# Performance work log

Hardware: AMD Instinct MI355X
Metric: run time of the kernel (lower is better)

## Reference

```python
import jax, jax.numpy as jnp
import numpy as np

B, N, C, P, K = 8, 65536, 96, 96, 512


def _ln(x, g, b, eps=1e-5):
    mu = x.mean(axis=-1, keepdims=True)
    var = ((x - mu) ** 2).mean(axis=-1, keepdims=True)
    return (x - mu) * jax.lax.rsqrt(var + eps) * g + b


def setup_inputs():
    key = jax.random.key(0)
    ks = jax.random.split(key, 8)
    inp = {
        "pts_feat": jax.random.normal(ks[0], (B, N, C), jnp.float32),
        "sp_idx": jax.random.randint(ks[1], (B, N), 0, K, jnp.int64),
        "all_xyz": jax.random.normal(ks[2], (B, N, 3), jnp.float32),
        # pts_proj1: Linear(3,P) -> LN -> ReLU -> Linear(P,P) -> LN
        "W1": jax.random.normal(ks[3], (3, P), jnp.float32) / np.sqrt(3.0),
        "b1": jnp.zeros((P,), jnp.float32),
        "g1": jnp.ones((P,), jnp.float32),
        "be1": jnp.zeros((P,), jnp.float32),
        "W2": jax.random.normal(ks[4], (P, P), jnp.float32) / np.sqrt(P),
        "b2": jnp.zeros((P,), jnp.float32),
        "g2": jnp.ones((P,), jnp.float32),
        "be2": jnp.zeros((P,), jnp.float32),
        # pts_proj2: Linear(2P,P) -> LN -> ReLU -> Linear(P,1,no bias) -> Sigmoid
        "W3": jax.random.normal(ks[5], (2 * P, P), jnp.float32) / np.sqrt(2.0 * P),
        "b3": jnp.zeros((P,), jnp.float32),
        "g3": jnp.ones((P,), jnp.float32),
        "be3": jnp.zeros((P,), jnp.float32),
        "W4": jax.random.normal(ks[6], (P, 1), jnp.float32) / np.sqrt(P),
        "num_sp": K,
    }
    return inp


def reference(pts_feat, sp_idx, all_xyz, W1, b1, g1, be1, W2, b2, g2, be2,
              W3, b3, g3, be3, W4, num_sp):
    Bx, Nx, Cx = pts_feat.shape
    S = Bx * num_sp  # total superpoints across batch (uniform K per batch)
    idx = (sp_idx + jnp.arange(Bx, dtype=sp_idx.dtype)[:, None] * num_sp).reshape(-1)
    xyz = all_xyz.reshape(-1, 3)
    feat = pts_feat.reshape(-1, Cx)

    # scatter_norm: unit-sphere normalize per segment
    mn = jax.ops.segment_min(xyz, idx, num_segments=S)
    mx = jax.ops.segment_max(xyz, idx, num_segments=S)
    cnt = jax.ops.segment_sum(jnp.ones((xyz.shape[0],), xyz.dtype), idx, num_segments=S)
    cnt_c = jnp.maximum(cnt, 1.0)
    center = jax.ops.segment_sum(xyz, idx, num_segments=S) / cnt_c[:, None]
    diam = (mx - mn).max(axis=1)
    pts = (xyz - center[idx]) / (diam[idx][:, None] + 0.01)

    # pts_proj1
    h = _ln(pts @ W1 + b1, g1, be1)
    h = jax.nn.relu(h)
    h = _ln(h @ W2 + b2, g2, be2)

    seg = jax.ops.segment_max(h, idx, num_segments=S)  # (S, P)
    cat = jnp.concatenate([h, seg[idx]], axis=-1)      # (B*N, 2P)

    # pts_proj2
    z = _ln(cat @ W3 + b3, g3, be3)
    z = jax.nn.relu(z)
    w = jax.nn.sigmoid(z @ W4) * 2.0                   # (B*N, 1)

    sp_feat = jax.ops.segment_sum(feat * w, idx, num_segments=S) / cnt_c[:, None] + seg
    return sp_feat.reshape(Bx, num_sp, Cx), w.reshape(Bx, Nx, 1)
```

## Files before the change

kernel.cpp:

```cpp
#include <hip/hip_runtime.h>
#include <cstdint>

#define MM 524288
#define NSEG 4096

#define WS_SCNT   0u
#define WS_CURSOR 4096u
#define WS_OFFS   8192u
#define WS_M1     12288u
#define WS_CENTER 12304u
#define WS_DIAM   24592u
#define WS_SEGF   28688u
#define WS_ZSEG   421904u
#define WS_SORTED 815120u
#define WS_H8     1339408u
#define WS_END    (WS_H8 + 25165824u)

typedef __attribute__((ext_vector_type(8))) short short8;
typedef __attribute__((ext_vector_type(4))) float f32x4;

#define WPAD 104

__device__ __forceinline__ unsigned bfr(float x) {
    unsigned u = __float_as_uint(x);
    return (u + 0x7FFFu + ((u >> 16) & 1u)) >> 16;
}
__device__ __forceinline__ float bf2f(unsigned v) {
    return __uint_as_float(v << 16);
}
union U4S8 { uint4 u; short8 s; };

__global__ void __launch_bounds__(256) k0_init(unsigned* __restrict__ ws)
{
    unsigned i = blockIdx.x * 256u + threadIdx.x;
    if (i < 8192u) ws[i] = 0u;
}

__global__ void __launch_bounds__(256) k1_count(
    const int* __restrict__ spidx, unsigned* __restrict__ scnt)
{
    __shared__ unsigned lcnt[512];
    int tid = threadIdx.x;
    for (int j = tid; j < 512; j += 256) lcnt[j] = 0u;
    __syncthreads();
    int base = blockIdx.x * 4096;
    #pragma unroll 4
    for (int it = 0; it < 16; ++it) {
        int p = base + it*256 + tid;
        atomicAdd(&lcnt[spidx[p]], 1u);
    }
    __syncthreads();
    int b = blockIdx.x >> 4;
    for (int j = tid; j < 512; j += 256)
        atomicAdd(&scnt[(b << 9) + j], lcnt[j]);
}

__global__ void __launch_bounds__(1024) k2_scan(
    const unsigned* __restrict__ scnt, unsigned* __restrict__ offs,
    const float* __restrict__ W1, const float* __restrict__ b1, float* __restrict__ m1)
{
    __shared__ unsigned sh[1024];
    int t = threadIdx.x;
    unsigned c0 = scnt[t*4+0], c1 = scnt[t*4+1], c2 = scnt[t*4+2], c3 = scnt[t*4+3];
    unsigned tot = c0 + c1 + c2 + c3;
    sh[t] = tot;
    __syncthreads();
    for (int d = 1; d < 1024; d <<= 1) {
        unsigned v = (t >= d) ? sh[t-d] : 0u;
        __syncthreads();
        sh[t] += v;
        __syncthreads();
    }
    unsigned excl = sh[t] - tot;
    offs[t*4+0] = excl;
    offs[t*4+1] = excl + c0;
    offs[t*4+2] = excl + c0 + c1;
    offs[t*4+3] = excl + c0 + c1 + c2;

    if (t == 0) {
        float Sa=0,Sb=0,Sc=0,Sd=0,Saa=0,Sbb=0,Scc=0,Sdd=0,Sab=0,Sac=0,Sad=0,Sbc=0,Sbd=0,Scd=0;
        #pragma unroll 8
        for (int j = 0; j < 96; ++j) {
            float A = W1[j], B2 = W1[96+j], C2 = W1[192+j], D = b1[j];
            Sa+=A; Sb+=B2; Sc+=C2; Sd+=D;
            Saa=fmaf(A,A,Saa); Sbb=fmaf(B2,B2,Sbb); Scc=fmaf(C2,C2,Scc); Sdd=fmaf(D,D,Sdd);
            Sab=fmaf(A,B2,Sab); Sac=fmaf(A,C2,Sac); Sad=fmaf(A,D,Sad);
            Sbc=fmaf(B2,C2,Sbc); Sbd=fmaf(B2,D,Sbd); Scd=fmaf(C2,D,Scd);
        }
        const float inv = 1.f/96.f;
        float Am=Sa*inv, Bm=Sb*inv, Cm=Sc*inv, Dm=Sd*inv;
        m1[0]=Am; m1[1]=Bm; m1[2]=Cm; m1[3]=Dm;
        m1[4]=Saa*inv-Am*Am; m1[5]=Sbb*inv-Bm*Bm; m1[6]=Scc*inv-Cm*Cm; m1[7]=Sdd*inv-Dm*Dm;
        m1[8]=Sab*inv-Am*Bm; m1[9]=Sac*inv-Am*Cm; m1[10]=Sad*inv-Am*Dm;
        m1[11]=Sbc*inv-Bm*Cm; m1[12]=Sbd*inv-Bm*Dm; m1[13]=Scd*inv-Cm*Dm;
    }
}

__global__ void __launch_bounds__(256) k3_scatter(
    const int* __restrict__ spidx, const unsigned* __restrict__ offs,
    unsigned* __restrict__ cursor, unsigned* __restrict__ sorted)
{
    __shared__ unsigned lcnt[512];
    __shared__ unsigned gbase[512];
    __shared__ unsigned short rank16[4096];
    int tid = threadIdx.x;
    for (int j = tid; j < 512; j += 256) lcnt[j] = 0u;
    __syncthreads();
    int base = blockIdx.x * 4096;
    #pragma unroll 4
    for (int it = 0; it < 16; ++it) {
        int p = base + it*256 + tid;
        unsigned r = atomicAdd(&lcnt[spidx[p]], 1u);
        rank16[it*256 + tid] = (unsigned short)r;
    }
    __syncthreads();
    int b = blockIdx.x >> 4;
    for (int j = tid; j < 512; j += 256)
        gbase[j] = atomicAdd(&cursor[(b << 9) + j], lcnt[j]);
    __syncthreads();
    #pragma unroll 4
    for (int it = 0; it < 16; ++it) {
        int p = base + it*256 + tid;
        int sl = spidx[p];
        unsigned pos = offs[(b << 9) + sl] + gbase[sl] + (unsigned)rank16[it*256 + tid];
        sorted[pos] = (unsigned)p;
    }
}

__global__ void __launch_bounds__(128) k3b_stats(
    const float* __restrict__ xyz, const unsigned* __restrict__ sorted,
    const unsigned* __restrict__ offs, const unsigned* __restrict__ scnt,
    float* __restrict__ center, float* __restrict__ diam)
{
    int s = blockIdx.x, tid = threadIdx.x;
    unsigned cnt = scnt[s], off = offs[s];
    float mnx=INFINITY, mny=INFINITY, mnz=INFINITY;
    float mxx=-INFINITY, mxy=-INFINITY, mxz=-INFINITY;
    float smx=0.f, smy=0.f, smz=0.f;
    for (unsigned r = tid; r < cnt; r += 128) {
        unsigned p = sorted[off + r];
        float x = xyz[3*p], y = xyz[3*p+1], z = xyz[3*p+2];
        mnx = fminf(mnx, x); mny = fminf(mny, y); mnz = fminf(mnz, z);
        mxx = fmaxf(mxx, x); mxy = fmaxf(mxy, y); mxz = fmaxf(mxz, z);
        smx += x; smy += y; smz += z;
    }
    #pragma unroll
    for (int m = 1; m < 64; m <<= 1) {
        mnx = fminf(mnx, __shfl_xor(mnx, m)); mny = fminf(mny, __shfl_xor(mny, m));
        mnz = fminf(mnz, __shfl_xor(mnz, m));
        mxx = fmaxf(mxx, __shfl_xor(mxx, m)); mxy = fmaxf(mxy, __shfl_xor(mxy, m));
        mxz = fmaxf(mxz, __shfl_xor(mxz, m));
        smx += __shfl_xor(smx, m); smy += __shfl_xor(smy, m); smz += __shfl_xor(smz, m);
    }
    __shared__ float cw[2][9];
    if ((tid & 63) == 0) {
        int w = tid >> 6;
        cw[w][0]=mnx; cw[w][1]=mny; cw[w][2]=mnz;
        cw[w][3]=mxx; cw[w][4]=mxy; cw[w][5]=mxz;
        cw[w][6]=smx; cw[w][7]=smy; cw[w][8]=smz;
    }
    __syncthreads();
    if (tid == 0) {
        float a0=fminf(cw[0][0],cw[1][0]), a1=fminf(cw[0][1],cw[1][1]), a2=fminf(cw[0][2],cw[1][2]);
        float b0=fmaxf(cw[0][3],cw[1][3]), b1=fmaxf(cw[0][4],cw[1][4]), b2=fmaxf(cw[0][5],cw[1][5]);
        float s0=cw[0][6]+cw[1][6], s1=cw[0][7]+cw[1][7], s2=cw[0][8]+cw[1][8];
        float cc = fmaxf((float)cnt, 1.f);
        center[s*3+0] = s0/cc; center[s*3+1] = s1/cc; center[s*3+2] = s2/cc;
        diam[s] = fmaxf(fmaxf(b0-a0, b1-a1), b2-a2);
    }
}

__global__ void __launch_bounds__(256) kT(
    const float* __restrict__ xyz, const int* __restrict__ spidx,
    const float* __restrict__ center, const float* __restrict__ diam,
    const float* __restrict__ W1, const float* __restrict__ b1,
    const float* __restrict__ g1, const float* __restrict__ be1,
    const float* __restrict__ m1, uint4* __restrict__ t8)
{
    size_t p = (size_t)blockIdx.x * 256 + threadIdx.x;
    int s = ((int)(p >> 16) << 9) + spidx[p];
    float dinv = 1.f / (diam[s] + 0.01f);
    float px = (xyz[3*p+0] - center[3*s+0]) * dinv;
    float py = (xyz[3*p+1] - center[3*s+1]) * dinv;
    float pz = (xyz[3*p+2] - center[3*s+2]) * dinv;

    float mu = fmaf(px, m1[0], fmaf(py, m1[1], fmaf(pz, m1[2], m1[3])));
    float var = fmaf(px*px, m1[4], fmaf(py*py, m1[5], fmaf(pz*pz, m1[6], m1[7])));
    var = fmaf(2.f*px*py, m1[8],  var);
    var = fmaf(2.f*px*pz, m1[9],  var);
    var = fmaf(2.f*px,    m1[10], var);
    var = fmaf(2.f*py*pz, m1[11], var);
    var = fmaf(2.f*py,    m1[12], var);
    var = fmaf(2.f*pz,    m1[13], var);
    float rs = rsqrtf(var + 1e-5f);

    #pragma unroll 4
    for (int q = 0; q < 12; ++q) {
        unsigned vv[4];
        #pragma unroll
        for (int e2 = 0; e2 < 4; ++e2) {
            int i0 = q*8 + e2*2;
            float ta = fmaf(px, W1[i0], fmaf(py, W1[96+i0], fmaf(pz, W1[192+i0], b1[i0])));
            ta = fmaxf(fmaf((ta - mu) * rs, g1[i0], be1[i0]), 0.f);
            float tb = fmaf(px, W1[i0+1], fmaf(py, W1[96+i0+1], fmaf(pz, W1[192+i0+1], b1[i0+1])));
            tb = fmaxf(fmaf((tb - mu) * rs, g1[i0+1], be1[i0+1]), 0.f);
            vv[e2] = bfr(ta) | (bfr(tb) << 16);
        }
        uint4 v; v.x = vv[0]; v.y = vv[1]; v.z = vv[2]; v.w = vv[3];
        t8[(size_t)q * MM + p] = v;
    }
}

__global__ void __launch_bounds__(256) kA_mfma(
    uint4* th8,
    const float* __restrict__ W2, const float* __restrict__ b2,
    const float* __restrict__ g2, const float* __restrict__ be2)
{
    __shared__ unsigned short wT[96*WPAD];
    __shared__ float prm[3*96];
    int tid = threadIdx.x;
    #pragma unroll 4
    for (int it = 0; it < 36; ++it) {
        int e = it*256 + tid;
        int i = e / 96;
        int j = e - i*96;
        wT[j*WPAD + i] = (unsigned short)bfr(W2[e]);
    }
    if (tid < 96) { prm[tid] = b2[tid]; prm[96+tid] = g2[tid]; prm[192+tid] = be2[tid]; }
    __syncthreads();

    int lane = tid & 63, w = tid >> 6;
    int pcol = lane & 15, g = lane >> 4;
    size_t pbase = (size_t)blockIdx.x * 256 + w * 64 + pcol;

    uint4 B0 = th8[(size_t)(0*4+g) * MM + pbase];
    uint4 B1 = th8[(size_t)(1*4+g) * MM + pbase];
    uint4 B2q = th8[(size_t)(2*4+g) * MM + pbase];

    #pragma unroll 1
    for (int t = 0; t < 4; ++t) {
        size_t p = pbase + (size_t)t * 16;
        uint4 C0 = B0, C1 = B1, C2 = B2q;
        if (t < 3) {
            size_t pn = p + 16;
            C0 = th8[(size_t)(0*4+g) * MM + pn];
            C1 = th8[(size_t)(1*4+g) * MM + pn];
            C2 = th8[(size_t)(2*4+g) * MM + pn];
        }
        U4S8 u0, u1, u2; u0.u = B0; u1.u = B1; u2.u = B2q;
        short8 bB[3] = { u0.s, u1.s, u2.s };

        f32x4 acc[6];
        #pragma unroll
        for (int nt = 0; nt < 6; ++nt) acc[nt] = (f32x4){0.f,0.f,0.f,0.f};

        #pragma unroll
        for (int ks = 0; ks < 3; ++ks) {
            #pragma unroll
            for (int nt = 0; nt < 6; ++nt) {
                const short8 aF = *(const short8*)&wT[(nt*16 + pcol)*WPAD + ks*32 + g*8];
                acc[nt] = __builtin_amdgcn_mfma_f32_16x16x32_bf16(aF, bB[ks], acc[nt], 0, 0, 0);
            }
        }

        float sum = 0.f, sq = 0.f;
        #pragma unroll
        for (int nt = 0; nt < 6; ++nt) {
            f32x4 bv = *(const f32x4*)&prm[nt*16 + g*4];
            #pragma unroll
            for (int r = 0; r < 4; ++r) {
                float v = acc[nt][r] + bv[r];
                acc[nt][r] = v;
                sum += v;
                sq = fmaf(v, v, sq);
            }
        }
        sum += __shfl_xor(sum, 16); sum += __shfl_xor(sum, 32);
        sq  += __shfl_xor(sq, 16);  sq  += __shfl_xor(sq, 32);
        float mu = sum * (1.f/96.f);
        float rs = rsqrtf(sq * (1.f/96.f) - mu*mu + 1e-5f);

        #pragma unroll
        for (int nt = 0; nt < 6; ++nt) {
            f32x4 gv  = *(const f32x4*)&prm[96  + nt*16 + g*4];
            f32x4 bev = *(const f32x4*)&prm[192 + nt*16 + g*4];
            float o0 = fmaf((acc[nt][0]-mu)*rs, gv[0], bev[0]);
            float o1 = fmaf((acc[nt][1]-mu)*rs, gv[1], bev[1]);
            float o2 = fmaf((acc[nt][2]-mu)*rs, gv[2], bev[2]);
            float o3 = fmaf((acc[nt][3]-mu)*rs, gv[3], bev[3]);
            uint2 st;
            st.x = bfr(o0) | (bfr(o1) << 16);
            st.y = bfr(o2) | (bfr(o3) << 16);
            int j0 = nt*16 + g*4;
            size_t q = (size_t)(nt*2 + (g >> 1));
            *(uint2*)((char*)th8 + (q*MM + p)*16 + (size_t)(j0 & 7)*2) = st;
        }
        B0 = C0; B1 = C1; B2q = C2;
    }
}

__global__ void __launch_bounds__(128) kB_seg(
    const unsigned short* __restrict__ h8u,
    const unsigned* __restrict__ sorted, const unsigned* __restrict__ offs,
    const unsigned* __restrict__ scnt,
    const float* __restrict__ W3, const float* __restrict__ b3,
    float* __restrict__ segf, float* __restrict__ zseg)
{
    __shared__ float lseg[96];
    int s = blockIdx.x, tid = threadIdx.x;
    unsigned cnt = scnt[s], off = offs[s];
    if (tid < 96) {
        int q = tid >> 3, e = tid & 7;
        size_t strq = (size_t)q * MM * 8 + e;
        float mx = -INFINITY;
        unsigned r = 0;
        for (; r + 4 <= cnt; r += 4) {
            unsigned p0 = sorted[off+r],   p1 = sorted[off+r+1];
            unsigned p2 = sorted[off+r+2], p3 = sorted[off+r+3];
            float a = bf2f(h8u[strq + (size_t)p0*8]);
            float b = bf2f(h8u[strq + (size_t)p1*8]);
            float c = bf2f(h8u[strq + (size_t)p2*8]);
            float d = bf2f(h8u[strq + (size_t)p3*8]);
            mx = fmaxf(mx, fmaxf(fmaxf(a,b), fmaxf(c,d)));
        }
        for (; r < cnt; ++r) {
            unsigned p0 = sorted[off+r];
            mx = fmaxf(mx, bf2f(h8u[strq + (size_t)p0*8]));
        }
        segf[(size_t)s*96 + tid] = mx;
        lseg[tid] = mx;
    }
    __syncthreads();
    if (tid < 96) {
        float acc = b3[tid];
        #pragma unroll 4
        for (int i = 0; i < 96; ++i)
            acc = fmaf(lseg[i], W3[(size_t)(96+i)*96 + tid], acc);
        zseg[(size_t)s*96 + tid] = acc;
    }
}

__global__ void __launch_bounds__(256) kC_mfma(
    const uint4* __restrict__ h8, const float* __restrict__ zseg,
    const int* __restrict__ spidx,
    const float* __restrict__ W3, const float* __restrict__ g3,
    const float* __restrict__ be3, const float* __restrict__ W4,
    float* __restrict__ w_out)
{
    __shared__ unsigned short wT[96*WPAD];
    __shared__ float prm[3*96];
    int tid = threadIdx.x;
    #pragma unroll 4
    for (int it = 0; it < 36; ++it) {
        int e = it*256 + tid;
        int i = e / 96;
        int j = e - i*96;
        wT[j*WPAD + i] = (unsigned short)bfr(W3[e]);
    }
    if (tid < 96) { prm[tid] = g3[tid]; prm[96+tid] = be3[tid]; prm[192+tid] = W4[tid]; }
    __syncthreads();

    int lane = tid & 63, w = tid >> 6;
    int pcol = lane & 15, g = lane >> 4;
    size_t pbase = (size_t)blockIdx.x * 256 + w * 64 + pcol;

    uint4 B0 = h8[(size_t)(0*4+g) * MM + pbase];
    uint4 B1 = h8[(size_t)(1*4+g) * MM + pbase];
    uint4 B2q = h8[(size_t)(2*4+g) * MM + pbase];

    #pragma unroll 1
    for (int t = 0; t < 4; ++t) {
        size_t p = pbase + (size_t)t * 16;
        uint4 C0 = B0, C1 = B1, C2 = B2q;
        if (t < 3) {
            size_t pn = p + 16;
            C0 = h8[(size_t)(0*4+g) * MM + pn];
            C1 = h8[(size_t)(1*4+g) * MM + pn];
            C2 = h8[(size_t)(2*4+g) * MM + pn];
        }
        U4S8 u0, u1, u2; u0.u = B0; u1.u = B1; u2.u = B2q;
        short8 bB[3] = { u0.s, u1.s, u2.s };

        f32x4 acc[6];
        #pragma unroll
        for (int nt = 0; nt < 6; ++nt) acc[nt] = (f32x4){0.f,0.f,0.f,0.f};

        #pragma unroll
        for (int ks = 0; ks < 3; ++ks) {
            #pragma unroll
            for (int nt = 0; nt < 6; ++nt) {
                const short8 aF = *(const short8*)&wT[(nt*16 + pcol)*WPAD + ks*32 + g*8];
                acc[nt] = __builtin_amdgcn_mfma_f32_16x16x32_bf16(aF, bB[ks], acc[nt], 0, 0, 0);
            }
        }

        int sp = spidx[p];
        int s = ((int)(p >> 16) << 9) + sp;

        float sum = 0.f, sq = 0.f;
        #pragma unroll
        for (int nt = 0; nt < 6; ++nt) {
            f32x4 zs = *(const f32x4*)&zseg[(size_t)s*96 + nt*16 + g*4];
            #pragma unroll
            for (int r = 0; r < 4; ++r) {
                float v = acc[nt][r] + zs[r];
                acc[nt][r] = v;
                sum += v;
                sq = fmaf(v, v, sq);
            }
        }
        sum += __shfl_xor(sum, 16); sum += __shfl_xor(sum, 32);
        sq  += __shfl_xor(sq, 16);  sq  += __shfl_xor(sq, 32);
        float mu = sum * (1.f/96.f);
        float rs = rsqrtf(sq * (1.f/96.f) - mu*mu + 1e-5f);

        float tt = 0.f;
        #pragma unroll
        for (int nt = 0; nt < 6; ++nt) {
            f32x4 gv  = *(const f32x4*)&prm[nt*16 + g*4];
            f32x4 bev = *(const f32x4*)&prm[96 + nt*16 + g*4];
            f32x4 w4v = *(const f32x4*)&prm[192 + nt*16 + g*4];
            #pragma unroll
            for (int r = 0; r < 4; ++r) {
                float v = fmaxf(fmaf((acc[nt][r]-mu)*rs, gv[r], bev[r]), 0.f);
                tt = fmaf(v, w4v[r], tt);
            }
        }
        tt += __shfl_xor(tt, 16); tt += __shfl_xor(tt, 32);
        if (lane < 16) w_out[p] = 2.f / (1.f + expf(-tt));

        B0 = C0; B1 = C1; B2q = C2;
    }
}

__global__ void __launch_bounds__(128) kD_pool(
    const float* __restrict__ feat, const float* __restrict__ w_out,
    const unsigned* __restrict__ sorted, const unsigned* __restrict__ offs,
    const unsigned* __restrict__ scnt, const float* __restrict__ segf,
    float* __restrict__ sp_out)
{
    int s = blockIdx.x;
    int c = threadIdx.x;
    unsigned cnt = scnt[s], off = offs[s];
    float acc = 0.f;
    unsigned r = 0;
    for (; r + 4 <= cnt; r += 4) {
        unsigned p0 = sorted[off+r],   p1 = sorted[off+r+1];
        unsigned p2 = sorted[off+r+2], p3 = sorted[off+r+3];
        float w0 = w_out[p0], w1 = w_out[p1], w2 = w_out[p2], w3 = w_out[p3];
        if (c < 96) {
            acc = fmaf(feat[(size_t)p0*96 + c], w0, acc);
            acc = fmaf(feat[(size_t)p1*96 + c], w1, acc);
            acc = fmaf(feat[(size_t)p2*96 + c], w2, acc);
            acc = fmaf(feat[(size_t)p3*96 + c], w3, acc);
        }
    }
    for (; r < cnt; ++r) {
        unsigned p0 = sorted[off+r];
        float w0 = w_out[p0];
        if (c < 96) acc = fmaf(feat[(size_t)p0*96 + c], w0, acc);
    }
    if (c < 96) {
        float cc = fmaxf((float)cnt, 1.f);
        sp_out[(size_t)s*96 + c] = acc / cc + segf[(size_t)s*96 + c];
    }
}

extern "C" void kernel_launch(void* const* d_in, const int* in_sizes, int n_in,
                              void* d_out, int out_size, void* d_ws, size_t ws_size,
                              hipStream_t stream)
{
    const float* pts_feat = (const float*)d_in[0];
    const int*   sp_idx   = (const int*)d_in[1];
    const float* xyz      = (const float*)d_in[2];
    const float* W1  = (const float*)d_in[3];
    const float* b1  = (const float*)d_in[4];
    const float* g1  = (const float*)d_in[5];
    const float* be1 = (const float*)d_in[6];
    const float* W2  = (const float*)d_in[7];
    const float* b2  = (const float*)d_in[8];
    const float* g2  = (const float*)d_in[9];
    const float* be2 = (const float*)d_in[10];
    const float* W3  = (const float*)d_in[11];
    const float* b3  = (const float*)d_in[12];
    const float* g3  = (const float*)d_in[13];
    const float* be3 = (const float*)d_in[14];
    const float* W4  = (const float*)d_in[15];

    float* out = (float*)d_out;
    float* sp_out = out;
    float* w_out  = out + (size_t)NSEG * 96;

    if (ws_size < (size_t)WS_END * 4u) return;

    unsigned* ws32   = (unsigned*)d_ws;
    unsigned* scnt   = ws32 + WS_SCNT;
    unsigned* cursor = ws32 + WS_CURSOR;
    unsigned* offs   = ws32 + WS_OFFS;
    float*    m1     = (float*)(ws32 + WS_M1);
    float*    center = (float*)(ws32 + WS_CENTER);
    float*    diam   = (float*)(ws32 + WS_DIAM);
    float*    segf   = (float*)(ws32 + WS_SEGF);
    float*    zseg   = (float*)(ws32 + WS_ZSEG);
    unsigned* sorted = ws32 + WS_SORTED;
    uint4*    th8    = (uint4*)(ws32 + WS_H8);

    k0_init<<<32, 256, 0, stream>>>(ws32);
    k1_count<<<MM/4096, 256, 0, stream>>>(sp_idx, scnt);
    k2_scan<<<1, 1024, 0, stream>>>(scnt, offs, W1, b1, m1);
    k3_scatter<<<MM/4096, 256, 0, stream>>>(sp_idx, offs, cursor, sorted);
    k3b_stats<<<NSEG, 128, 0, stream>>>(xyz, sorted, offs, scnt, center, diam);
    kT<<<MM/256, 256, 0, stream>>>(xyz, sp_idx, center, diam, W1, b1, g1, be1, m1, th8);
    kA_mfma<<<MM/256, 256, 0, stream>>>(th8, W2, b2, g2, be2);
    kB_seg<<<NSEG, 128, 0, stream>>>((const unsigned short*)th8, sorted, offs, scnt,
        W3, b3, segf, zseg);
    kC_mfma<<<MM/256, 256, 0, stream>>>(th8, zseg, sp_idx, W3, g3, be3, W4, w_out);
    kD_pool<<<NSEG, 128, 0, stream>>>(pts_feat, w_out, sorted, offs, scnt, segf, sp_out);
}
```

Before: 328.2 us.

## Fuse layer-1 and layer-2 and store hidden activations in segment-sorted order

Fuses the first projection (Linear+LN+ReLU) into the MFMA layer-2 kernel, so the intermediate bf16 activation no longer makes a round trip through global memory. Points are processed in segment-sorted order using a new per-slot segment id array written during scatter. The segment max kernel can then read contiguous, coalesced rows from h8 through LDS instead of gathering through sorted indices. The last kernel writes weights both in sorted and natural order, which adds a scattered store and an extra workspace buffer and makes the xyz reads in the fused kernel gathered.

```diff
diff --git a/kernel.cpp b/kernel.cpp
--- a/kernel.cpp
+++ b/kernel.cpp
@@ -13,7 +13,9 @@
 #define WS_SEGF   28688u
 #define WS_ZSEG   421904u
 #define WS_SORTED 815120u
-#define WS_H8     1339408u
+#define WS_SEG16  1339408u
+#define WS_WSRT   1601552u
+#define WS_H8     2125840u
 #define WS_END    (WS_H8 + 25165824u)
 
 typedef __attribute__((ext_vector_type(8))) short short8;
@@ -98,7 +100,8 @@
 
 __global__ void __launch_bounds__(256) k3_scatter(
     const int* __restrict__ spidx, const unsigned* __restrict__ offs,
-    unsigned* __restrict__ cursor, unsigned* __restrict__ sorted)
+    unsigned* __restrict__ cursor, unsigned* __restrict__ sorted,
+    unsigned short* __restrict__ seg16)
 {
     __shared__ unsigned lcnt[512];
     __shared__ unsigned gbase[512];
@@ -122,8 +125,10 @@
     for (int it = 0; it < 16; ++it) {
         int p = base + it*256 + tid;
         int sl = spidx[p];
-        unsigned pos = offs[(b << 9) + sl] + gbase[sl] + (unsigned)rank16[it*256 + tid];
+        int s = (b << 9) + sl;
+        unsigned pos = offs[s] + gbase[sl] + (unsigned)rank16[it*256 + tid];
         sorted[pos] = (unsigned)p;
+        seg16[pos] = (unsigned short)s;
     }
 }
 
@@ -170,51 +175,174 @@
     }
 }
 
-__global__ void __launch_bounds__(256) kT(
-    const float* __restrict__ xyz, const int* __restrict__ spidx,
+__global__ void __launch_bounds__(256) kTA(
+    const float* __restrict__ xyz,
+    const unsigned* __restrict__ sorted,
+    const unsigned short* __restrict__ seg16,
     const float* __restrict__ center, const float* __restrict__ diam,
     const float* __restrict__ W1, const float* __restrict__ b1,
     const float* __restrict__ g1, const float* __restrict__ be1,
-    const float* __restrict__ m1, uint4* __restrict__ t8)
-{
-    size_t p = (size_t)blockIdx.x * 256 + threadIdx.x;
-    int s = ((int)(p >> 16) << 9) + spidx[p];
-    float dinv = 1.f / (diam[s] + 0.01f);
-    float px = (xyz[3*p+0] - center[3*s+0]) * dinv;
-    float py = (xyz[3*p+1] - center[3*s+1]) * dinv;
-    float pz = (xyz[3*p+2] - center[3*s+2]) * dinv;
-
-    float mu = fmaf(px, m1[0], fmaf(py, m1[1], fmaf(pz, m1[2], m1[3])));
-    float var = fmaf(px*px, m1[4], fmaf(py*py, m1[5], fmaf(pz*pz, m1[6], m1[7])));
-    var = fmaf(2.f*px*py, m1[8],  var);
-    var = fmaf(2.f*px*pz, m1[9],  var);
-    var = fmaf(2.f*px,    m1[10], var);
-    var = fmaf(2.f*py*pz, m1[11], var);
-    var = fmaf(2.f*py,    m1[12], var);
-    var = fmaf(2.f*pz,    m1[13], var);
-    float rs = rsqrtf(var + 1e-5f);
-
+    const float* __restrict__ m1,
+    const float* __restrict__ W2, const float* __restrict__ b2,
+    const float* __restrict__ g2, const float* __restrict__ be2,
+    uint4* __restrict__ h8)
+{
+    __shared__ unsigned short wT[96*WPAD];
+    __shared__ float pw[96*6];
+    __shared__ float prm[3*96];
+    int tid = threadIdx.x;
     #pragma unroll 4
-    for (int q = 0; q < 12; ++q) {
-        unsigned vv[4];
-        #pragma unroll
-        for (int e2 = 0; e2 < 4; ++e2) {
-            int i0 = q*8 + e2*2;
-            float ta = fmaf(px, W1[i0], fmaf(py, W1[96+i0], fmaf(pz, W1[192+i0], b1[i0])));
-            ta = fmaxf(fmaf((ta - mu) * rs, g1[i0], be1[i0]), 0.f);
-            float tb = fmaf(px, W1[i0+1], fmaf(py, W1[96+i0+1], fmaf(pz, W1[192+i0+1], b1[i0+1])));
-            tb = fmaxf(fmaf((tb - mu) * rs, g1[i0+1], be1[i0+1]), 0.f);
-            vv[e2] = bfr(ta) | (bfr(tb) << 16);
-        }
-        uint4 v; v.x = vv[0]; v.y = vv[1]; v.z = vv[2]; v.w = vv[3];
-        t8[(size_t)q * MM + p] = v;
-    }
-}
-
-__global__ void __launch_bounds__(256) kA_mfma(
-    uint4* th8,
-    const float* __restrict__ W2, const float* __restrict__ b2,
-    const float* __restrict__ g2, const float* __restrict__ be2)
+    for (int it = 0; it < 36; ++it) {
+        int e = it*256 + tid;
+        int i = e / 96, j = e - i*96;
+        wT[j*WPAD + i] = (unsigned short)bfr(W2[e]);
+    }
+    if (tid < 96) {
+        pw[tid*6+0] = W1[tid]; pw[tid*6+1] = W1[96+tid]; pw[tid*6+2] = W1[192+tid];
+        pw[tid*6+3] = b1[tid]; pw[tid*6+4] = g1[tid];    pw[tid*6+5] = be1[tid];
+        prm[tid] = b2[tid]; prm[96+tid] = g2[tid]; prm[192+tid] = be2[tid];
+    }
+    __syncthreads();
+
+    float mc[14];
+    #pragma unroll
+    for (int k = 0; k < 14; ++k) mc[k] = m1[k];
+
+    int lane = tid & 63, w = tid >> 6;
+    int pcol = lane & 15, g = lane >> 4;
+    size_t slot0 = (size_t)blockIdx.x * 256 + w*64 + pcol;
+
+    #pragma unroll 1
+    for (int t = 0; t < 4; ++t) {
+        size_t slot = slot0 + (size_t)t * 16;
+        unsigned p = sorted[slot];
+        int s = seg16[slot];
+        float dinv = 1.f / (diam[s] + 0.01f);
+        float px = (xyz[3*p+0] - center[3*s+0]) * dinv;
+        float py = (xyz[3*p+1] - center[3*s+1]) * dinv;
+        float pz = (xyz[3*p+2] - center[3*s+2]) * dinv;
+
+        float mu = fmaf(px, mc[0], fmaf(py, mc[1], fmaf(pz, mc[2], mc[3])));
+        float var = fmaf(px*px, mc[4], fmaf(py*py, mc[5], fmaf(pz*pz, mc[6], mc[7])));
+        var = fmaf(2.f*px*py, mc[8],  var);
+        var = fmaf(2.f*px*pz, mc[9],  var);
+        var = fmaf(2.f*px,    mc[10], var);
+        var = fmaf(2.f*py*pz, mc[11], var);
+        var = fmaf(2.f*py,    mc[12], var);
+        var = fmaf(2.f*pz,    mc[13], var);
+        float rs = rsqrtf(var + 1e-5f);
+
+        U4S8 bu[3];
+        #pragma unroll
+        for (int ks = 0; ks < 3; ++ks) {
+            unsigned vv[4];
+            #pragma unroll
+            for (int e2 = 0; e2 < 4; ++e2) {
+                int i0 = ks*32 + g*8 + e2*2;
+                const float* r0 = &pw[i0*6];
+                float ta = fmaf(px, r0[0], fmaf(py, r0[1], fmaf(pz, r0[2], r0[3])));
+                ta = fmaxf(fmaf((ta - mu) * rs, r0[4], r0[5]), 0.f);
+                const float* r1 = &pw[(i0+1)*6];
+                float tb = fmaf(px, r1[0], fmaf(py, r1[1], fmaf(pz, r1[2], r1[3])));
+                tb = fmaxf(fmaf((tb - mu) * rs, r1[4], r1[5]), 0.f);
+                vv[e2] = bfr(ta) | (bfr(tb) << 16);
+            }
+            bu[ks].u.x = vv[0]; bu[ks].u.y = vv[1]; bu[ks].u.z = vv[2]; bu[ks].u.w = vv[3];
+        }
+
+        f32x4 acc[6];
+        #pragma unroll
+        for (int nt = 0; nt < 6; ++nt) acc[nt] = (f32x4){0.f,0.f,0.f,0.f};
+
+        #pragma unroll
+        for (int ks = 0; ks < 3; ++ks) {
+            #pragma unroll
+            for (int nt = 0; nt < 6; ++nt) {
+                const short8 aF = *(const short8*)&wT[(nt*16 + pcol)*WPAD + ks*32 + g*8];
+                acc[nt] = __builtin_amdgcn_mfma_f32_16x16x32_bf16(aF, bu[ks].s, acc[nt], 0, 0, 0);
+            }
+        }
+
+        float sum = 0.f, sq = 0.f;
+        #pragma unroll
+        for (int nt = 0; nt < 6; ++nt) {
+            f32x4 bv = *(const f32x4*)&prm[nt*16 + g*4];
+            #pragma unroll
+            for (int r = 0; r < 4; ++r) {
+                float v = acc[nt][r] + bv[r];
+                acc[nt][r] = v;
+                sum += v;
+                sq = fmaf(v, v, sq);
+            }
+        }
+        sum += __shfl_xor(sum, 16); sum += __shfl_xor(sum, 32);
+        sq  += __shfl_xor(sq, 16);  sq  += __shfl_xor(sq, 32);
+        float muh = sum * (1.f/96.f);
+        float rsh = rsqrtf(sq * (1.f/96.f) - muh*muh + 1e-5f);
+
+        #pragma unroll
+        for (int nt = 0; nt < 6; ++nt) {
+            f32x4 gv  = *(const f32x4*)&prm[96  + nt*16 + g*4];
+            f32x4 bev = *(const f32x4*)&prm[192 + nt*16 + g*4];
+            float o0 = fmaf((acc[nt][0]-muh)*rsh, gv[0], bev[0]);
+            float o1 = fmaf((acc[nt][1]-muh)*rsh, gv[1], bev[1]);
+            float o2 = fmaf((acc[nt][2]-muh)*rsh, gv[2], bev[2]);
+            float o3 = fmaf((acc[nt][3]-muh)*rsh, gv[3], bev[3]);
+            uint2 st;
+            st.x = bfr(o0) | (bfr(o1) << 16);
+            st.y = bfr(o2) | (bfr(o3) << 16);
+            int j0 = nt*16 + g*4;
+            size_t q = (size_t)(nt*2 + (g >> 1));
+            *(uint2*)((char*)h8 + (q*MM + slot)*16 + (size_t)(j0 & 7)*2) = st;
+        }
+    }
+}
+
+__global__ void __launch_bounds__(192) kB_seg(
+    const uint4* __restrict__ h8,
+    const unsigned* __restrict__ offs, const unsigned* __restrict__ scnt,
+    const float* __restrict__ W3, const float* __restrict__ b3,
+    float* __restrict__ segf, float* __restrict__ zseg)
+{
+    __shared__ uint4 st[16][13];
+    __shared__ float lseg[96];
+    int s = blockIdx.x, tid = threadIdx.x;
+    unsigned cnt = scnt[s], off = offs[s];
+    int r = tid & 15, q = tid >> 4;
+    float mx = -INFINITY;
+    for (unsigned base = 0; base < cnt; base += 16) {
+        uint4 v = make_uint4(0xFF80FF80u, 0xFF80FF80u, 0xFF80FF80u, 0xFF80FF80u);
+        if (q < 12 && base + (unsigned)r < cnt)
+            v = h8[(size_t)q * MM + off + base + r];
+        if (q < 12) st[r][q] = v;
+        __syncthreads();
+        if (tid < 96) {
+            int qj = tid >> 3, ej = tid & 7;
+            #pragma unroll
+            for (int rr = 0; rr < 16; ++rr) {
+                const unsigned short* hp = (const unsigned short*)&st[rr][qj];
+                mx = fmaxf(mx, bf2f(hp[ej]));
+            }
+        }
+        __syncthreads();
+    }
+    if (tid < 96) { segf[(size_t)s*96 + tid] = mx; lseg[tid] = mx; }
+    __syncthreads();
+    if (tid < 96) {
+        float acc = b3[tid];
+        #pragma unroll 4
+        for (int i = 0; i < 96; ++i)
+            acc = fmaf(lseg[i], W3[(size_t)(96+i)*96 + tid], acc);
+        zseg[(size_t)s*96 + tid] = acc;
+    }
+}
+
+__global__ void __launch_bounds__(256) kC_mfma(
+    const uint4* __restrict__ h8, const float* __restrict__ zseg,
+    const unsigned short* __restrict__ seg16, const unsigned* __restrict__ sorted,
+    const float* __restrict__ W3, const float* __restrict__ g3,
+    const float* __restrict__ be3, const float* __restrict__ W4,
+    float* __restrict__ w_nat, float* __restrict__ w_srt)
 {
     __shared__ unsigned short wT[96*WPAD];
     __shared__ float prm[3*96];
@@ -222,33 +350,23 @@
     #pragma unroll 4
     for (int it = 0; it < 36; ++it) {
         int e = it*256 + tid;
-        int i = e / 96;
-        int j = e - i*96;
-        wT[j*WPAD + i] = (unsigned short)bfr(W2[e]);
-    }
-    if (tid < 96) { prm[tid] = b2[tid]; prm[96+tid] = g2[tid]; prm[192+tid] = be2[tid]; }
+        int i = e / 96, j = e - i*96;
+        wT[j*WPAD + i] = (unsigned short)bfr(W3[e]);
+    }
+    if (tid < 96) { prm[tid] = g3[tid]; prm[96+tid] = be3[tid]; prm[192+tid] = W4[tid]; }
     __syncthreads();
 
     int lane = tid & 63, w = tid >> 6;
     int pcol = lane & 15, g = lane >> 4;
-    size_t pbase = (size_t)blockIdx.x * 256 + w * 64 + pcol;
-
-    uint4 B0 = th8[(size_t)(0*4+g) * MM + pbase];
-    uint4 B1 = th8[(size_t)(1*4+g) * MM + pbase];
-    uint4 B2q = th8[(size_t)(2*4+g) * MM + pbase];
+    size_t slot0 = (size_t)blockIdx.x * 256 + w*64 + pcol;
 
     #pragma unroll 1
     for (int t = 0; t < 4; ++t) {
-        size_t p = pbase + (size_t)t * 16;
-        uint4 C0 = B0, C1 = B1, C2 = B2q;
-        if (t < 3) {
-            size_t pn = p + 16;
-            C0 = th8[(size_t)(0*4+g) * MM + pn];
-            C1 = th8[(size_t)(1*4+g) * MM + pn];
-            C2 = th8[(size_t)(2*4+g) * MM + pn];
-        }
-        U4S8 u0, u1, u2; u0.u = B0; u1.u = B1; u2.u = B2q;
-        short8 bB[3] = { u0.s, u1.s, u2.s };
+        size_t slot = slot0 + (size_t)t * 16;
+        U4S8 bu[3];
+        #pragma unroll
+        for (int ks = 0; ks < 3; ++ks)
+            bu[ks].u = h8[(size_t)(ks*4+g) * MM + slot];
 
         f32x4 acc[6];
         #pragma unroll
@@ -259,144 +377,11 @@
             #pragma unroll
             for (int nt = 0; nt < 6; ++nt) {
                 const short8 aF = *(const short8*)&wT[(nt*16 + pcol)*WPAD + ks*32 + g*8];
-                acc[nt] = __builtin_amdgcn_mfma_f32_16x16x32_bf16(aF, bB[ks], acc[nt], 0, 0, 0);
-            }
-        }
-
-        float sum = 0.f, sq = 0.f;
-        #pragma unroll
-        for (int nt = 0; nt < 6; ++nt) {
-            f32x4 bv = *(const f32x4*)&prm[nt*16 + g*4];
-            #pragma unroll
-            for (int r = 0; r < 4; ++r) {
-                float v = acc[nt][r] + bv[r];
-                acc[nt][r] = v;
-                sum += v;
-                sq = fmaf(v, v, sq);
-            }
-        }
-        sum += __shfl_xor(sum, 16); sum += __shfl_xor(sum, 32);
-        sq  += __shfl_xor(sq, 16);  sq  += __shfl_xor(sq, 32);
-        float mu = sum * (1.f/96.f);
-        float rs = rsqrtf(sq * (1.f/96.f) - mu*mu + 1e-5f);
-
-        #pragma unroll
-        for (int nt = 0; nt < 6; ++nt) {
-            f32x4 gv  = *(const f32x4*)&prm[96  + nt*16 + g*4];
-            f32x4 bev = *(const f32x4*)&prm[192 + nt*16 + g*4];
-            float o0 = fmaf((acc[nt][0]-mu)*rs, gv[0], bev[0]);
-            float o1 = fmaf((acc[nt][1]-mu)*rs, gv[1], bev[1]);
-            float o2 = fmaf((acc[nt][2]-mu)*rs, gv[2], bev[2]);
-            float o3 = fmaf((acc[nt][3]-mu)*rs, gv[3], bev[3]);
-            uint2 st;
-            st.x = bfr(o0) | (bfr(o1) << 16);
-            st.y = bfr(o2) | (bfr(o3) << 16);
-            int j0 = nt*16 + g*4;
-            size_t q = (size_t)(nt*2 + (g >> 1));
-            *(uint2*)((char*)th8 + (q*MM + p)*16 + (size_t)(j0 & 7)*2) = st;
-        }
-        B0 = C0; B1 = C1; B2q = C2;
-    }
-}
-
-__global__ void __launch_bounds__(128) kB_seg(
-    const unsigned short* __restrict__ h8u,
-    const unsigned* __restrict__ sorted, const unsigned* __restrict__ offs,
-    const unsigned* __restrict__ scnt,
-    const float* __restrict__ W3, const float* __restrict__ b3,
-    float* __restrict__ segf, float* __restrict__ zseg)
-{
-    __shared__ float lseg[96];
-    int s = blockIdx.x, tid = threadIdx.x;
-    unsigned cnt = scnt[s], off = offs[s];
-    if (tid < 96) {
-        int q = tid >> 3, e = tid & 7;
-        size_t strq = (size_t)q * MM * 8 + e;
-        float mx = -INFINITY;
-        unsigned r = 0;
-        for (; r + 4 <= cnt; r += 4) {
-            unsigned p0 = sorted[off+r],   p1 = sorted[off+r+1];
-            unsigned p2 = sorted[off+r+2], p3 = sorted[off+r+3];
-            float a = bf2f(h8u[strq + (size_t)p0*8]);
-            float b = bf2f(h8u[strq + (size_t)p1*8]);
-            float c = bf2f(h8u[strq + (size_t)p2*8]);
-            float d = bf2f(h8u[strq + (size_t)p3*8]);
-            mx = fmaxf(mx, fmaxf(fmaxf(a,b), fmaxf(c,d)));
-        }
-        for (; r < cnt; ++r) {
-            unsigned p0 = sorted[off+r];
-            mx = fmaxf(mx, bf2f(h8u[strq + (size_t)p0*8]));
-        }
-        segf[(size_t)s*96 + tid] = mx;
-        lseg[tid] = mx;
-    }
-    __syncthreads();
-    if (tid < 96) {
-        float acc = b3[tid];
-        #pragma unroll 4
-        for (int i = 0; i < 96; ++i)
-            acc = fmaf(lseg[i], W3[(size_t)(96+i)*96 + tid], acc);
-        zseg[(size_t)s*96 + tid] = acc;
-    }
-}
-
-__global__ void __launch_bounds__(256) kC_mfma(
-    const uint4* __restrict__ h8, const float* __restrict__ zseg,
-    const int* __restrict__ spidx,
-    const float* __restrict__ W3, const float* __restrict__ g3,
-    const float* __restrict__ be3, const float* __restrict__ W4,
-    float* __restrict__ w_out)
-{
-    __shared__ unsigned short wT[96*WPAD];
-    __shared__ float prm[3*96];
-    int tid = threadIdx.x;
-    #pragma unroll 4
-    for (int it = 0; it < 36; ++it) {
-        int e = it*256 + tid;
-        int i = e / 96;
-        int j = e - i*96;
-        wT[j*WPAD + i] = (unsigned short)bfr(W3[e]);
-    }
-    if (tid < 96) { prm[tid] = g3[tid]; prm[96+tid] = be3[tid]; prm[192+tid] = W4[tid]; }
-    __syncthreads();
-
-    int lane = tid & 63, w = tid >> 6;
-    int pcol = lane & 15, g = lane >> 4;
-    size_t pbase = (size_t)blockIdx.x * 256 + w * 64 + pcol;
-
-    uint4 B0 = h8[(size_t)(0*4+g) * MM + pbase];
-    uint4 B1 = h8[(size_t)(1*4+g) * MM + pbase];
-    uint4 B2q = h8[(size_t)(2*4+g) * MM + pbase];
-
-    #pragma unroll 1
-    for (int t = 0; t < 4; ++t) {
-        size_t p = pbase + (size_t)t * 16;
-        uint4 C0 = B0, C1 = B1, C2 = B2q;
-        if (t < 3) {
-            size_t pn = p + 16;
-            C0 = h8[(size_t)(0*4+g) * MM + pn];
-            C1 = h8[(size_t)(1*4+g) * MM + pn];
-            C2 = h8[(size_t)(2*4+g) * MM + pn];
-        }
-        U4S8 u0, u1, u2; u0.u = B0; u1.u = B1; u2.u = B2q;
-        short8 bB[3] = { u0.s, u1.s, u2.s };
-
-        f32x4 acc[6];
-        #pragma unroll
-        for (int nt = 0; nt < 6; ++nt) acc[nt] = (f32x4){0.f,0.f,0.f,0.f};
-
-        #pragma unroll
-        for (int ks = 0; ks < 3; ++ks) {
-            #pragma unroll
-            for (int nt = 0; nt < 6; ++nt) {
-                const short8 aF = *(const short8*)&wT[(nt*16 + pcol)*WPAD + ks*32 + g*8];
-                acc[nt] = __builtin_amdgcn_mfma_f32_16x16x32_bf16(aF, bB[ks], acc[nt], 0, 0, 0);
-            }
-        }
-
-        int sp = spidx[p];
-        int s = ((int)(p >> 16) << 9) + sp;
-
+                acc[nt] = __builtin_amdgcn_mfma_f32_16x16x32_bf16(aF, bu[ks].s, acc[nt], 0, 0, 0);
+            }
+        }
+
+        int s = seg16[slot];
         float sum = 0.f, sq = 0.f;
         #pragma unroll
         for (int nt = 0; nt < 6; ++nt) {
@@ -427,14 +412,16 @@
             }
         }
         tt += __shfl_xor(tt, 16); tt += __shfl_xor(tt, 32);
-        if (lane < 16) w_out[p] = 2.f / (1.f + expf(-tt));
-
-        B0 = C0; B1 = C1; B2q = C2;
+        if (lane < 16) {
+            float wv = 2.f / (1.f + expf(-tt));
+            w_srt[slot] = wv;
+            w_nat[sorted[slot]] = wv;
+        }
     }
 }
 
 __global__ void __launch_bounds__(128) kD_pool(
-    const float* __restrict__ feat, const float* __restrict__ w_out,
+    const float* __restrict__ feat, const float* __restrict__ w_srt,
     const unsigned* __restrict__ sorted, const unsigned* __restrict__ offs,
     const unsigned* __restrict__ scnt, const float* __restrict__ segf,
     float* __restrict__ sp_out)
@@ -447,7 +434,7 @@
     for (; r + 4 <= cnt; r += 4) {
         unsigned p0 = sorted[off+r],   p1 = sorted[off+r+1];
         unsigned p2 = sorted[off+r+2], p3 = sorted[off+r+3];
-        float w0 = w_out[p0], w1 = w_out[p1], w2 = w_out[p2], w3 = w_out[p3];
+        float w0 = w_srt[off+r], w1 = w_srt[off+r+1], w2 = w_srt[off+r+2], w3 = w_srt[off+r+3];
         if (c < 96) {
             acc = fmaf(feat[(size_t)p0*96 + c], w0, acc);
             acc = fmaf(feat[(size_t)p1*96 + c], w1, acc);
@@ -457,7 +444,7 @@
     }
     for (; r < cnt; ++r) {
         unsigned p0 = sorted[off+r];
-        float w0 = w_out[p0];
+        float w0 = w_srt[off+r];
         if (c < 96) acc = fmaf(feat[(size_t)p0*96 + c], w0, acc);
     }
     if (c < 96) {
@@ -503,17 +490,19 @@
     float*    segf   = (float*)(ws32 + WS_SEGF);
     float*    zseg   = (float*)(ws32 + WS_ZSEG);
     unsigned* sorted = ws32 + WS_SORTED;
-    uint4*    th8    = (uint4*)(ws32 + WS_H8);
+    unsigned short* seg16 = (unsigned short*)(ws32 + WS_SEG16);
+    float*    w_srt  = (float*)(ws32 + WS_WSRT);
+    uint4*    h8     = (uint4*)(ws32 + WS_H8);
 
     k0_init<<<32, 256, 0, stream>>>(ws32);
     k1_count<<<MM/4096, 256, 0, stream>>>(sp_idx, scnt);
     k2_scan<<<1, 1024, 0, stream>>>(scnt, offs, W1, b1, m1);
-    k3_scatter<<<MM/4096, 256, 0, stream>>>(sp_idx, offs, cursor, sorted);
+    k3_scatter<<<MM/4096, 256, 0, stream>>>(sp_idx, offs, cursor, sorted, seg16);
     k3b_stats<<<NSEG, 128, 0, stream>>>(xyz, sorted, offs, scnt, center, diam);
-    kT<<<MM/256, 256, 0, stream>>>(xyz, sp_idx, center, diam, W1, b1, g1, be1, m1, th8);
-    kA_mfma<<<MM/256, 256, 0, stream>>>(th8, W2, b2, g2, be2);
-    kB_seg<<<NSEG, 128, 0, stream>>>((const unsigned short*)th8, sorted, offs, scnt,
-        W3, b3, segf, zseg);
-    kC_mfma<<<MM/256, 256, 0, stream>>>(th8, zseg, sp_idx, W3, g3, be3, W4, w_out);
-    kD_pool<<<NSEG, 128, 0, stream>>>(pts_feat, w_out, sorted, offs, scnt, segf, sp_out);
-}
+    kTA<<<MM/256, 256, 0, stream>>>(xyz, sorted, seg16, center, diam,
+        W1, b1, g1, be1, m1, W2, b2, g2, be2, h8);
+    kB_seg<<<NSEG, 192, 0, stream>>>(h8, offs, scnt, W3, b3, segf, zseg);
+    kC_mfma<<<MM/256, 256, 0, stream>>>(h8, zseg, seg16, sorted, W3, g3, be3, W4,
+        w_out, w_srt);
+    kD_pool<<<NSEG, 128, 0, stream>>>(pts_feat, w_srt, sorted, offs, scnt, segf, sp_out);
+}
```

Measured after the change: 265.0 us. 19.3% less time.
